# Optimization experiments

Measured on AMD Instinct MI355X. Metric: run time of the kernel, lower is better.

The kernel has to match this reference:

```python
import jax, jax.numpy as jnp
import numpy as np

N_NODES = 24


def _gcn_adj(edge_index):
    # PyG GCNConv normalization: add self-loops, deg over target nodes,
    # norm = deg^{-1/2}[src] * deg^{-1/2}[dst], aggregate out[dst] += norm * x[src].
    src = jnp.concatenate([edge_index[0], jnp.arange(N_NODES)])
    dst = jnp.concatenate([edge_index[1], jnp.arange(N_NODES)])
    ones = jnp.ones(src.shape[0], dtype=jnp.float32)
    deg = jax.ops.segment_sum(ones, dst, num_segments=N_NODES)
    dinv = 1.0 / jnp.sqrt(deg)  # deg >= 1 thanks to self-loops
    norm = dinv[src] * dinv[dst]
    # Dense normalized adjacency (24x24 is trivially small); A @ x == scatter-add of norm*x[src] into dst
    return jnp.zeros((N_NODES, N_NODES), dtype=jnp.float32).at[dst, src].add(norm)


def setup_inputs() -> dict:
    key = jax.random.key(0)
    ks = jax.random.split(key, 24)
    B, F0 = 32768, 1
    dims = [F0, 4, 4, 8, 8, 16, 16, 32]
    inp = {
        "x": jax.random.normal(ks[0], (B, N_NODES, F0), dtype=jnp.float32),
        "edge_index": jax.random.randint(ks[1], (2, 96), 0, N_NODES, dtype=jnp.int64),
    }
    for i in range(7):
        fin, fout = dims[i], dims[i + 1]
        s = 1.0 / np.sqrt(fin)
        inp[f"W{i+1}"] = jax.random.uniform(ks[2 + 2 * i], (fin, fout), minval=-s, maxval=s, dtype=jnp.float32)
        inp[f"b{i+1}"] = jnp.zeros((fout,), dtype=jnp.float32)
    inp["fcw1"] = jax.random.uniform(ks[16], (768, 128), minval=-1 / np.sqrt(768), maxval=1 / np.sqrt(768), dtype=jnp.float32)
    inp["fcb1"] = jnp.zeros((128,), dtype=jnp.float32)
    inp["fcw2"] = jax.random.uniform(ks[17], (128, 2), minval=-1 / np.sqrt(128), maxval=1 / np.sqrt(128), dtype=jnp.float32)
    inp["fcb2"] = jnp.zeros((2,), dtype=jnp.float32)
    return inp


def reference(x, edge_index, W1, b1, W2, b2, W3, b3, W4, b4, W5, b5, W6, b6, W7, b7, fcw1, fcb1, fcw2, fcb2):
    A = _gcn_adj(edge_index)  # [24, 24]
    h = x  # [B, 24, F]
    for W, b in ((W1, b1), (W2, b2), (W3, b3), (W4, b4), (W5, b5), (W6, b6), (W7, b7)):
        h = jax.nn.relu(jnp.einsum("ij,bjf->bif", A, h @ W) + b)
    h = h.reshape(h.shape[0], -1)  # [B, 768]
    h = h @ fcw1 + fcb1  # no activation between fc1 and fc2 in the original
    h = h @ fcw2 + fcb2  # [B, 2]
    return jax.nn.log_softmax(h, axis=-1)
```

## Files before the change

### kernel.cpp

```cpp
#include <hip/hip_runtime.h>
#include <math.h>

#define NN   24
#define EPB  16
#define CSTR 24
#define ESTR 388
#define T    256
#define AT_OFF 2176

typedef float v2f __attribute__((ext_vector_type(2)));
typedef float v4f __attribute__((ext_vector_type(4)));

static __device__ __forceinline__ v2f pkfma(v2f a, v2f b, v2f c) {
  asm("v_pk_fma_f32 %0, %1, %2, %0" : "+v"(c) : "v"(a), "v"(b));
  return c;
}
static __device__ __forceinline__ v2f pkfma_b0(v2f a, v2f b, v2f c) {
  asm("v_pk_fma_f32 %0, %1, %2, %0 op_sel:[0,0,0] op_sel_hi:[1,0,1]"
      : "+v"(c) : "v"(a), "v"(b));
  return c;
}
static __device__ __forceinline__ v2f pkfma_b1(v2f a, v2f b, v2f c) {
  asm("v_pk_fma_f32 %0, %1, %2, %0 op_sel:[0,1,0] op_sel_hi:[1,1,1]"
      : "+v"(c) : "v"(a), "v"(b));
  return c;
}
static __device__ __forceinline__ v2f pkfma_sb0(v2f a, v2f b, v2f c) {
  asm("v_pk_fma_f32 %0, %1, %2, %0 op_sel:[0,0,0] op_sel_hi:[1,0,1]"
      : "+v"(c) : "s"(a), "v"(b));
  return c;
}
static __device__ __forceinline__ v2f pkfma_sb1(v2f a, v2f b, v2f c) {
  asm("v_pk_fma_f32 %0, %1, %2, %0 op_sel:[0,1,0] op_sel_hi:[1,1,1]"
      : "+v"(c) : "s"(a), "v"(b));
  return c;
}


__global__ void prep_kernel(const int* __restrict__ ei, int ec,
                            const float* __restrict__ fcw1, const float* __restrict__ fcb1,
                            const float* __restrict__ fcw2, const float* __restrict__ fcb2,
                            float* __restrict__ ws) {
  int t = threadIdx.x;
  if (blockIdx.x == 0) {
    __shared__ float deg[NN];
    __shared__ float dinv[NN];
    __shared__ float As[NN*NN];
    __shared__ int s_is64;
    if (t == 0) s_is64 = 1;
    if (t < NN) deg[t] = 1.0f;
    for (int k = t; k < NN*NN; k += T) As[k] = 0.0f;
    __syncthreads();
    for (int k = t; k < 2*ec; k += T) {
      if (ei[2*k + 1] != 0) atomicExch(&s_is64, 0);
    }
    __syncthreads();
    int is64 = s_is64;
    for (int k = t; k < ec; k += T) {
      int d = is64 ? ei[2*(ec + k)] : ei[ec + k];
      atomicAdd(&deg[d], 1.0f);
    }
    __syncthreads();
    if (t < NN) dinv[t] = 1.0f / sqrtf(deg[t]);
    __syncthreads();
    for (int k = t; k < ec; k += T) {
      int s = is64 ? ei[2*k]        : ei[k];
      int d = is64 ? ei[2*(ec + k)] : ei[ec + k];
      atomicAdd(&As[d*NN + s], dinv[s]*dinv[d]);
    }
    if (t < NN) atomicAdd(&As[t*NN + t], dinv[t]*dinv[t]);
    __syncthreads();
    for (int k = t; k < NN*NN; k += T) {
      float a = As[k];
      int r = k / NN, c = k % NN;
      ws[k] = a;
      ws[AT_OFF + c*NN + r] = a;
    }
    if (t < 2) {
      float acc = fcb2[t];
      for (int k = 0; k < 128; ++k) acc += fcb1[k]*fcw2[k*2 + t];
      ws[2112 + t] = acc;
    }
  } else {
    __shared__ __align__(16) float w2t[256];
    for (int k = t; k < 256; k += T) w2t[(k & 1)*128 + (k >> 1)] = fcw2[k];
    __syncthreads();
    int r0 = (blockIdx.x - 1) * 96;
    for (int idx = t; idx < 96*2; idx += T) {
      int r = r0 + (idx >> 1), c = idx & 1;
      const v4f* w1r = (const v4f*)(fcw1 + r*128);
      const v4f* w2v = (const v4f*)(w2t + c*128);
      v4f s = (v4f){0.f, 0.f, 0.f, 0.f};
      #pragma unroll
      for (int k = 0; k < 32; ++k) s = w1r[k]*w2v[k] + s;
      ws[576 + r*2 + c] = (s.x + s.y) + (s.z + s.w);
    }
  }
}

template<int FIN, int FOUT, int SPLIT>
__device__ __forceinline__ void merged_layer(const float* __restrict__ ATg,
                                             const float* Ash, float* gbuf,
                                             const float* Ws, const float* bs, int t) {
  constexpr int NCOLS = EPB*FOUT;
  constexpr int CL    = NN/SPLIT;
  constexpr int NV    = CL/2;
  constexpr int KS    = (CL == 6) ? 2 : (CL == 12 ? 4 : 8);
  int col = t & (NCOLS - 1);
  int i0  = __builtin_amdgcn_readfirstlane((t / NCOLS) * CL);
  int e = col / FOUT;
  int f = col & (FOUT - 1);
  const float* ib = gbuf + e*ESTR;
  float wcol[FIN];
  #pragma unroll
  for (int fi = 0; fi < FIN; ++fi) wcol[fi] = Ws[fi*FOUT + f];
  float bf = bs[f];
  v2f hh[12];
  #pragma unroll
  for (int k = 0; k < 12; ++k) hh[k] = (v2f){bf, bf};
  #pragma unroll
  for (int fi = 0; fi < FIN; ++fi) {
    v2f w2 = (v2f){wcol[fi], wcol[fi]};
    const v4f* c4 = (const v4f*)(ib + fi*CSTR);
    #pragma unroll
    for (int k = 0; k < 6; ++k) {
      v4f v = c4[k];
      v2f lo = __builtin_shufflevector(v, v, 0, 1);
      v2f hi = __builtin_shufflevector(v, v, 2, 3);
      hh[2*k]   = pkfma(lo, w2, hh[2*k]);
      hh[2*k+1] = pkfma(hi, w2, hh[2*k+1]);
    }
  }
  #pragma unroll
  for (int k = 0; k < 12; ++k)
    hh[k] = __builtin_elementwise_max(hh[k], (v2f){0.f, 0.f});
  __syncthreads();
  float* ob = gbuf + e*ESTR + f*CSTR + i0;
  v2f acc[NV] = {};
  #pragma unroll
  for (int jp = 0; jp < 12; ++jp) {
    v2f hp = hh[jp];
    const v2f* gA = (const v2f*)(ATg + (2*jp)*NN + i0);
    const v2f* gB = (const v2f*)(ATg + (2*jp + 1)*NN + i0);
    #pragma unroll
    for (int k = 0; k < KS; ++k) {
      acc[k] = pkfma_sb0(gA[k], hp, acc[k]);
      acc[k] = pkfma_sb1(gB[k], hp, acc[k]);
    }
    const float* lA = Ash + (2*jp)*NN + i0;
    const float* lB = Ash + (2*jp + 1)*NN + i0;
    if constexpr (CL == 6) {
      acc[2] = pkfma_b0(((const v2f*)lA)[2], hp, acc[2]);
      acc[2] = pkfma_b1(((const v2f*)lB)[2], hp, acc[2]);
    } else {
      constexpr int NQ = (NV - KS) / 2;
      const v4f* qA = (const v4f*)(lA + 2*KS);
      const v4f* qB = (const v4f*)(lB + 2*KS);
      #pragma unroll
      for (int q = 0; q < NQ; ++q) {
        v4f a4 = qA[q], b4 = qB[q];
        acc[KS+2*q]   = pkfma_b0(__builtin_shufflevector(a4,a4,0,1), hp, acc[KS+2*q]);
        acc[KS+2*q+1] = pkfma_b0(__builtin_shufflevector(a4,a4,2,3), hp, acc[KS+2*q+1]);
        acc[KS+2*q]   = pkfma_b1(__builtin_shufflevector(b4,b4,0,1), hp, acc[KS+2*q]);
        acc[KS+2*q+1] = pkfma_b1(__builtin_shufflevector(b4,b4,2,3), hp, acc[KS+2*q+1]);
      }
    }
  }
  #pragma unroll
  for (int k = 0; k < NV; ++k) *(v2f*)(ob + 2*k) = acc[k];
}

__global__ __launch_bounds__(256, 4) void gcn_main(
    const float* __restrict__ x, const float* __restrict__ ws,
    const float* __restrict__ W1, const float* __restrict__ b1,
    const float* __restrict__ W2, const float* __restrict__ b2,
    const float* __restrict__ W3, const float* __restrict__ b3,
    const float* __restrict__ W4, const float* __restrict__ b4,
    const float* __restrict__ W5, const float* __restrict__ b5,
    const float* __restrict__ W6, const float* __restrict__ b6,
    const float* __restrict__ W7, const float* __restrict__ b7,
    float* __restrict__ out) {
  __shared__ __align__(16) float gbuf[EPB*ESTR];
  __shared__ float Wsh[500];
  __shared__ __align__(16) float bsh[88];
  __shared__ __align__(16) float Ash[NN*NN];
  int t = threadIdx.x;
  const float* ATg = ws + AT_OFF;

  {
    const float* Wp[6] = {W1,W2,W3,W4,W5,W6};
    const float* bp[7] = {b1,b2,b3,b4,b5,b6,b7};
    const int wsz[6] = {4,16,32,64,128,256};
    const int wof[6] = {0,4,20,52,116,244};
    const int bsz[7] = {4,4,8,8,16,16,32};
    const int bof[7] = {0,4,8,16,24,40,56};
    #pragma unroll
    for (int l = 0; l < 6; ++l) {
      for (int k = t; k < wsz[l]; k += T) Wsh[wof[l] + k] = Wp[l][k];
    }
    #pragma unroll
    for (int l = 0; l < 7; ++l) {
      if (t < bsz[l]) bsh[bof[l] + t] = bp[l][t];
    }
  }
  if (t < NN*NN/4) ((v4f*)Ash)[t] = ((const v4f*)(ws + AT_OFF))[t];
  {
    const float* xg = x + (size_t)blockIdx.x * (EPB*NN);
    if (t < EPB*NN/4) {
      float4 v = ((const float4*)xg)[t];
      int e = t/6, k = t - e*6;
      ((float4*)(gbuf + e*ESTR + CSTR))[k] = v;
    }
  }
  __syncthreads();

  {
    int e = t & 15, i = t >> 4;
    const float4* xv = (const float4*)(gbuf + e*ESTR + CSTR);
    const float4* Ar = (const float4*)(ws + i*NN);
    float acc = 0.f;
    #pragma unroll
    for (int k = 0; k < 6; ++k) {
      float4 a = Ar[k]; float4 v = xv[k];
      acc += a.x*v.x + a.y*v.y + a.z*v.z + a.w*v.w;
    }
    gbuf[e*ESTR + i] = acc;
    if (t < 128) {
      int i2 = 16 + (t >> 4);
      const float4* Ar2 = (const float4*)(ws + i2*NN);
      float acc2 = 0.f;
      #pragma unroll
      for (int k = 0; k < 6; ++k) {
        float4 a = Ar2[k]; float4 v = xv[k];
        acc2 += a.x*v.x + a.y*v.y + a.z*v.z + a.w*v.w;
      }
      gbuf[e*ESTR + i2] = acc2;
    }
  }
  __syncthreads();

  merged_layer<1, 4, 4>(ATg, Ash, gbuf, Wsh+0,   bsh+0,  t); __syncthreads();
  merged_layer<4, 4, 4>(ATg, Ash, gbuf, Wsh+4,   bsh+4,  t); __syncthreads();
  merged_layer<4, 8, 2>(ATg, Ash, gbuf, Wsh+20,  bsh+8,  t); __syncthreads();
  merged_layer<8, 8, 2>(ATg, Ash, gbuf, Wsh+52,  bsh+16, t); __syncthreads();
  merged_layer<8,16, 1>(ATg, Ash, gbuf, Wsh+116, bsh+24, t); __syncthreads();
  merged_layer<16,16,1>(ATg, Ash, gbuf, Wsh+244, bsh+40, t); __syncthreads();

  {
    const float* Wc = ws + 576;
    float bc0 = ws[2112], bc1 = ws[2113];
    #pragma unroll
    for (int r = 0; r < 2; ++r) {
      int col = t + r*T;
      int e = col >> 5, f = col & 31;
      const float* ib = gbuf + e*ESTR;
      float bf = bsh[56 + f];
      v2f hh[12];
      #pragma unroll
      for (int k = 0; k < 12; ++k) hh[k] = (v2f){bf, bf};
      #pragma unroll
      for (int fi = 0; fi < 16; ++fi) {
        float w = W7[fi*32 + f];
        v2f w2 = (v2f){w, w};
        const v4f* c4 = (const v4f*)(ib + fi*CSTR);
        #pragma unroll
        for (int k = 0; k < 6; ++k) {
          v4f v = c4[k];
          v2f lo = __builtin_shufflevector(v, v, 0, 1);
          v2f hi = __builtin_shufflevector(v, v, 2, 3);
          hh[2*k]   = pkfma(lo, w2, hh[2*k]);
          hh[2*k+1] = pkfma(hi, w2, hh[2*k+1]);
        }
      }
      #pragma unroll
      for (int k = 0; k < 12; ++k)
        hh[k] = __builtin_elementwise_max(hh[k], (v2f){0.f, 0.f});
      v2f p = (v2f){0.f, 0.f};
      #pragma unroll
      for (int kp = 0; kp < 12; ++kp) {
        v2f hp = hh[kp];
        v2f wcA = *(const v2f*)(Wc + ((2*kp)*32 + f)*2);
        v2f wcB = *(const v2f*)(Wc + ((2*kp + 1)*32 + f)*2);
        p = pkfma_b0(wcA, hp, p);
        p = pkfma_b1(wcB, hp, p);
      }
      float p0 = p.x, p1 = p.y;
      #pragma unroll
      for (int m = 1; m < 32; m <<= 1) {
        p0 += __shfl_xor(p0, m, 32);
        p1 += __shfl_xor(p1, m, 32);
      }
      if (f < 2) {
        float z0 = p0 + bc0, z1 = p1 + bc1;
        float mx = fmaxf(z0, z1);
        float lse = mx + logf(expf(z0 - mx) + expf(z1 - mx));
        int eg = blockIdx.x*EPB + e;
        out[eg*2 + f] = (f == 0 ? z0 : z1) - lse;
      }
    }
  }
}

extern "C" void kernel_launch(void* const* d_in, const int* in_sizes, int n_in,
                              void* d_out, int out_size, void* d_ws, size_t ws_size,
                              hipStream_t stream) {
  const float* x    = (const float*)d_in[0];
  const int*   ei   = (const int*)  d_in[1];
  const float* W1   = (const float*)d_in[2];  const float* b1 = (const float*)d_in[3];
  const float* W2   = (const float*)d_in[4];  const float* b2 = (const float*)d_in[5];
  const float* W3   = (const float*)d_in[6];  const float* b3 = (const float*)d_in[7];
  const float* W4   = (const float*)d_in[8];  const float* b4 = (const float*)d_in[9];
  const float* W5   = (const float*)d_in[10]; const float* b5 = (const float*)d_in[11];
  const float* W6   = (const float*)d_in[12]; const float* b6 = (const float*)d_in[13];
  const float* W7   = (const float*)d_in[14]; const float* b7 = (const float*)d_in[15];
  const float* fcw1 = (const float*)d_in[16]; const float* fcb1 = (const float*)d_in[17];
  const float* fcw2 = (const float*)d_in[18]; const float* fcb2 = (const float*)d_in[19];
  float* out = (float*)d_out;
  float* ws  = (float*)d_ws;
  int ec = in_sizes[1] / 2;
  int B  = in_sizes[0] / NN;

  hipLaunchKernelGGL(prep_kernel, dim3(9), dim3(T), 0, stream,
                     ei, ec, fcw1, fcb1, fcw2, fcb2, ws);
  hipLaunchKernelGGL(gcn_main, dim3(B/EPB), dim3(T), 0, stream,
                     x, ws, W1,b1, W2,b2, W3,b3, W4,b4, W5,b5, W6,b6, W7,b7, out);
}
```

Baseline: 157.6 us.

## Give each wavefront its own elements and replace block barriers with wave-local LDS fences

Result: slower. 165.3 us (+4.9%).

```diff
diff --git a/kernel.cpp b/kernel.cpp
--- a/kernel.cpp
+++ b/kernel.cpp
@@ -34,6 +34,9 @@
   asm("v_pk_fma_f32 %0, %1, %2, %0 op_sel:[0,1,0] op_sel_hi:[1,1,1]"
       : "+v"(c) : "s"(a), "v"(b));
   return c;
+}
+static __device__ __forceinline__ void wave_lds_fence() {
+  asm volatile("s_waitcnt lgkmcnt(0)" ::: "memory");
 }
 
 
@@ -101,15 +104,15 @@
 template<int FIN, int FOUT, int SPLIT>
 __device__ __forceinline__ void merged_layer(const float* __restrict__ ATg,
                                              const float* Ash, float* gbuf,
-                                             const float* Ws, const float* bs, int t) {
-  constexpr int NCOLS = EPB*FOUT;
-  constexpr int CL    = NN/SPLIT;
-  constexpr int NV    = CL/2;
-  constexpr int KS    = (CL == 6) ? 2 : (CL == 12 ? 4 : 8);
-  int col = t & (NCOLS - 1);
-  int i0  = __builtin_amdgcn_readfirstlane((t / NCOLS) * CL);
-  int e = col / FOUT;
-  int f = col & (FOUT - 1);
+                                             const float* Ws, const float* bs,
+                                             int lane, int w) {
+  constexpr int NCw = 4*FOUT;
+  constexpr int CL  = NN/SPLIT;
+  constexpr int NV  = CL/2;
+  int col = lane & (NCw - 1);
+  int i0  = (lane / NCw) * CL;
+  int e   = (w << 2) + col / FOUT;
+  int f   = col & (FOUT - 1);
   const float* ib = gbuf + e*ESTR;
   float wcol[FIN];
   #pragma unroll
@@ -134,40 +137,61 @@
   #pragma unroll
   for (int k = 0; k < 12; ++k)
     hh[k] = __builtin_elementwise_max(hh[k], (v2f){0.f, 0.f});
-  __syncthreads();
   float* ob = gbuf + e*ESTR + f*CSTR + i0;
   v2f acc[NV] = {};
-  #pragma unroll
-  for (int jp = 0; jp < 12; ++jp) {
-    v2f hp = hh[jp];
-    const v2f* gA = (const v2f*)(ATg + (2*jp)*NN + i0);
-    const v2f* gB = (const v2f*)(ATg + (2*jp + 1)*NN + i0);
-    #pragma unroll
-    for (int k = 0; k < KS; ++k) {
-      acc[k] = pkfma_sb0(gA[k], hp, acc[k]);
-      acc[k] = pkfma_sb1(gB[k], hp, acc[k]);
-    }
-    const float* lA = Ash + (2*jp)*NN + i0;
-    const float* lB = Ash + (2*jp + 1)*NN + i0;
-    if constexpr (CL == 6) {
-      acc[2] = pkfma_b0(((const v2f*)lA)[2], hp, acc[2]);
-      acc[2] = pkfma_b1(((const v2f*)lB)[2], hp, acc[2]);
-    } else {
-      constexpr int NQ = (NV - KS) / 2;
-      const v4f* qA = (const v4f*)(lA + 2*KS);
-      const v4f* qB = (const v4f*)(lB + 2*KS);
-      #pragma unroll
-      for (int q = 0; q < NQ; ++q) {
+  if constexpr (SPLIT == 1) {
+    #pragma unroll
+    for (int jp = 0; jp < 12; ++jp) {
+      v2f hp = hh[jp];
+      const v2f* gA = (const v2f*)(ATg + (2*jp)*NN);
+      const v2f* gB = (const v2f*)(ATg + (2*jp + 1)*NN);
+      #pragma unroll
+      for (int k = 0; k < 8; ++k) {
+        acc[k] = pkfma_sb0(gA[k], hp, acc[k]);
+        acc[k] = pkfma_sb1(gB[k], hp, acc[k]);
+      }
+      const v4f* qA = (const v4f*)(Ash + (2*jp)*NN + 16);
+      const v4f* qB = (const v4f*)(Ash + (2*jp + 1)*NN + 16);
+      #pragma unroll
+      for (int q = 0; q < 2; ++q) {
         v4f a4 = qA[q], b4 = qB[q];
-        acc[KS+2*q]   = pkfma_b0(__builtin_shufflevector(a4,a4,0,1), hp, acc[KS+2*q]);
-        acc[KS+2*q+1] = pkfma_b0(__builtin_shufflevector(a4,a4,2,3), hp, acc[KS+2*q+1]);
-        acc[KS+2*q]   = pkfma_b1(__builtin_shufflevector(b4,b4,0,1), hp, acc[KS+2*q]);
-        acc[KS+2*q+1] = pkfma_b1(__builtin_shufflevector(b4,b4,2,3), hp, acc[KS+2*q+1]);
+        acc[8+2*q]   = pkfma_b0(__builtin_shufflevector(a4,a4,0,1), hp, acc[8+2*q]);
+        acc[8+2*q+1] = pkfma_b0(__builtin_shufflevector(a4,a4,2,3), hp, acc[8+2*q+1]);
+        acc[8+2*q]   = pkfma_b1(__builtin_shufflevector(b4,b4,0,1), hp, acc[8+2*q]);
+        acc[8+2*q+1] = pkfma_b1(__builtin_shufflevector(b4,b4,2,3), hp, acc[8+2*q+1]);
+      }
+    }
+  } else if constexpr (CL == 12) {
+    #pragma unroll
+    for (int jp = 0; jp < 12; ++jp) {
+      v2f hp = hh[jp];
+      const v4f* qA = (const v4f*)(Ash + (2*jp)*NN + i0);
+      const v4f* qB = (const v4f*)(Ash + (2*jp + 1)*NN + i0);
+      #pragma unroll
+      for (int q = 0; q < 3; ++q) {
+        v4f a4 = qA[q], b4 = qB[q];
+        acc[2*q]   = pkfma_b0(__builtin_shufflevector(a4,a4,0,1), hp, acc[2*q]);
+        acc[2*q+1] = pkfma_b0(__builtin_shufflevector(a4,a4,2,3), hp, acc[2*q+1]);
+        acc[2*q]   = pkfma_b1(__builtin_shufflevector(b4,b4,0,1), hp, acc[2*q]);
+        acc[2*q+1] = pkfma_b1(__builtin_shufflevector(b4,b4,2,3), hp, acc[2*q+1]);
+      }
+    }
+  } else {
+    #pragma unroll
+    for (int jp = 0; jp < 12; ++jp) {
+      v2f hp = hh[jp];
+      const v2f* at2A = (const v2f*)(Ash + (2*jp)*NN + i0);
+      const v2f* at2B = (const v2f*)(Ash + (2*jp + 1)*NN + i0);
+      #pragma unroll
+      for (int k = 0; k < 3; ++k) {
+        acc[k] = pkfma_b0(at2A[k], hp, acc[k]);
+        acc[k] = pkfma_b1(at2B[k], hp, acc[k]);
       }
     }
   }
   #pragma unroll
   for (int k = 0; k < NV; ++k) *(v2f*)(ob + 2*k) = acc[k];
+  wave_lds_fence();
 }
 
 __global__ __launch_bounds__(256, 4) void gcn_main(
@@ -185,6 +209,8 @@
   __shared__ __align__(16) float bsh[88];
   __shared__ __align__(16) float Ash[NN*NN];
   int t = threadIdx.x;
+  int lane = t & 63;
+  int w = t >> 6;
   const float* ATg = ws + AT_OFF;
 
   {
@@ -196,26 +222,28 @@
     const int bof[7] = {0,4,8,16,24,40,56};
     #pragma unroll
     for (int l = 0; l < 6; ++l) {
-      for (int k = t; k < wsz[l]; k += T) Wsh[wof[l] + k] = Wp[l][k];
+      for (int k = lane; k < wsz[l]; k += 64) Wsh[wof[l] + k] = Wp[l][k];
     }
     #pragma unroll
     for (int l = 0; l < 7; ++l) {
-      if (t < bsz[l]) bsh[bof[l] + t] = bp[l][t];
-    }
-  }
-  if (t < NN*NN/4) ((v4f*)Ash)[t] = ((const v4f*)(ws + AT_OFF))[t];
+      if (lane < bsz[l]) bsh[bof[l] + lane] = bp[l][lane];
+    }
+    for (int k = lane; k < NN*NN; k += 64) Ash[k] = ws[AT_OFF + k];
+  }
   {
     const float* xg = x + (size_t)blockIdx.x * (EPB*NN);
-    if (t < EPB*NN/4) {
-      float4 v = ((const float4*)xg)[t];
-      int e = t/6, k = t - e*6;
+    if (lane < 24) {
+      int idx = w*24 + lane;
+      float4 v = ((const float4*)xg)[idx];
+      int e = idx/6, k = idx - e*6;
       ((float4*)(gbuf + e*ESTR + CSTR))[k] = v;
     }
   }
-  __syncthreads();
+  wave_lds_fence();
 
   {
-    int e = t & 15, i = t >> 4;
+    int e = (w << 2) + (lane >> 4);
+    int i = lane & 15;
     const float4* xv = (const float4*)(gbuf + e*ESTR + CSTR);
     const float4* Ar = (const float4*)(ws + i*NN);
     float acc = 0.f;
@@ -225,34 +253,36 @@
       acc += a.x*v.x + a.y*v.y + a.z*v.z + a.w*v.w;
     }
     gbuf[e*ESTR + i] = acc;
-    if (t < 128) {
-      int i2 = 16 + (t >> 4);
+    if (lane < 32) {
+      int e2 = (w << 2) + (lane >> 3);
+      int i2 = 16 + (lane & 7);
+      const float4* xv2 = (const float4*)(gbuf + e2*ESTR + CSTR);
       const float4* Ar2 = (const float4*)(ws + i2*NN);
       float acc2 = 0.f;
       #pragma unroll
       for (int k = 0; k < 6; ++k) {
-        float4 a = Ar2[k]; float4 v = xv[k];
+        float4 a = Ar2[k]; float4 v = xv2[k];
         acc2 += a.x*v.x + a.y*v.y + a.z*v.z + a.w*v.w;
       }
-      gbuf[e*ESTR + i2] = acc2;
-    }
-  }
-  __syncthreads();
-
-  merged_layer<1, 4, 4>(ATg, Ash, gbuf, Wsh+0,   bsh+0,  t); __syncthreads();
-  merged_layer<4, 4, 4>(ATg, Ash, gbuf, Wsh+4,   bsh+4,  t); __syncthreads();
-  merged_layer<4, 8, 2>(ATg, Ash, gbuf, Wsh+20,  bsh+8,  t); __syncthreads();
-  merged_layer<8, 8, 2>(ATg, Ash, gbuf, Wsh+52,  bsh+16, t); __syncthreads();
-  merged_layer<8,16, 1>(ATg, Ash, gbuf, Wsh+116, bsh+24, t); __syncthreads();
-  merged_layer<16,16,1>(ATg, Ash, gbuf, Wsh+244, bsh+40, t); __syncthreads();
+      gbuf[e2*ESTR + i2] = acc2;
+    }
+  }
+  wave_lds_fence();
+
+  merged_layer<1, 4, 4>(ATg, Ash, gbuf, Wsh+0,   bsh+0,  lane, w);
+  merged_layer<4, 4, 4>(ATg, Ash, gbuf, Wsh+4,   bsh+4,  lane, w);
+  merged_layer<4, 8, 2>(ATg, Ash, gbuf, Wsh+20,  bsh+8,  lane, w);
+  merged_layer<8, 8, 2>(ATg, Ash, gbuf, Wsh+52,  bsh+16, lane, w);
+  merged_layer<8,16, 1>(ATg, Ash, gbuf, Wsh+116, bsh+24, lane, w);
+  merged_layer<16,16,1>(ATg, Ash, gbuf, Wsh+244, bsh+40, lane, w);
 
   {
     const float* Wc = ws + 576;
     float bc0 = ws[2112], bc1 = ws[2113];
     #pragma unroll
     for (int r = 0; r < 2; ++r) {
-      int col = t + r*T;
-      int e = col >> 5, f = col & 31;
+      int col = lane + r*64;
+      int e = (w << 2) + (col >> 5), f = col & 31;
       const float* ib = gbuf + e*ESTR;
       float bf = bsh[56 + f];
       v2f hh[12];
@@ -260,8 +290,8 @@
       for (int k = 0; k < 12; ++k) hh[k] = (v2f){bf, bf};
       #pragma unroll
       for (int fi = 0; fi < 16; ++fi) {
-        float w = W7[fi*32 + f];
-        v2f w2 = (v2f){w, w};
+        float ww = W7[fi*32 + f];
+        v2f w2 = (v2f){ww, ww};
         const v4f* c4 = (const v4f*)(ib + fi*CSTR);
         #pragma unroll
         for (int k = 0; k < 6; ++k) {
```
